# Kernel optimization log

Measured on AMD Instinct MI355X. Metric: run time of the kernel, lower is better.

The kernel has to match this reference:

```python
import jax, jax.numpy as jnp
import numpy as np
from jax import lax

N_NODES = 100000
N_EDGES = 6400000


def setup_inputs() -> dict:
    key = jax.random.key(0)
    k1, k2, k3, k4 = jax.random.split(key, 4)
    values = jax.random.uniform(k1, (N_NODES,), dtype=jnp.float32)
    edge_weights = jax.random.normal(k2, (N_EDGES,), dtype=jnp.float32)
    neighbor_idx = jax.random.randint(k3, (N_EDGES,), 0, N_NODES, dtype=jnp.int64 if jax.config.jax_enable_x64 else jnp.int32)
    segment_ids = jnp.sort(jax.random.randint(k4, (N_EDGES,), 0, N_NODES, dtype=jnp.int64 if jax.config.jax_enable_x64 else jnp.int32))
    return {
        "values": values,
        "edge_weights": edge_weights,
        "neighbor_idx": neighbor_idx,
        "segment_ids": segment_ids,
        "n_times": 3,
    }


def reference(values, edge_weights, neighbor_idx, segment_ids, n_times):
    # One forward_once: for each node i, new[i] = sigmoid(sum_{e: dst(e)=i} w_e * values[src(e)])
    # (per-node Linear(num_links, 1, bias=False) + Sigmoid, flattened over the ragged edge list)
    n_nodes = values.shape[0]

    def step(v, _):
        msgs = edge_weights * v[neighbor_idx]                      # [n_edges]
        agg = jax.ops.segment_sum(msgs, segment_ids, num_segments=n_nodes)
        return jax.nn.sigmoid(agg), None

    out, _ = lax.scan(step, values, None, length=int(n_times))
    return out
```

## Files before the change

kernel.cpp:

```cpp
#include <hip/hip_runtime.h>
#include <hip/hip_bf16.h>

#define BLK    512
#define EPT    16
#define CHUNK  24576
#define NPASS  5
#define CAP    (NPASS * CHUNK)
#define ROUNDS 6
#define SLOTS  640

__device__ __forceinline__ ushort f32_to_bf16_rne(float f) {
    unsigned u = __float_as_uint(f);
    unsigned r = (u + 0x7fffu + ((u >> 16) & 1u)) >> 16;
    return (ushort)r;
}

__global__ __launch_bounds__(BLK) void ppgcn_step(const ushort* __restrict__ vb,
                                                  const float* __restrict__ w,
                                                  const int* __restrict__ idx,
                                                  const int* __restrict__ seg,
                                                  float* __restrict__ acc,
                                                  int n_edges, int n_nodes) {
    __shared__ __align__(16) ushort chunk[CHUNK];
    __shared__ float slots[SLOTS];
    __shared__ int s_first, s_last;

    const int tid = threadIdx.x;
    const long long bstart = (long long)blockIdx.x * (BLK * EPT);
    const long long base   = bstart + (long long)tid * EPT;

    int ii[EPT]; float ww[EPT]; int ss[EPT];

    if (base + EPT <= (long long)n_edges) {
        const int4*   ip = reinterpret_cast<const int4*>(idx + base);
        const float4* wp = reinterpret_cast<const float4*>(w + base);
        const int4*   sp = reinterpret_cast<const int4*>(seg + base);
        #pragma unroll
        for (int q = 0; q < EPT / 4; ++q) {
            int4 a = ip[q]; float4 b = wp[q]; int4 c = sp[q];
            ii[4*q+0]=a.x; ii[4*q+1]=a.y; ii[4*q+2]=a.z; ii[4*q+3]=a.w;
            ww[4*q+0]=b.x; ww[4*q+1]=b.y; ww[4*q+2]=b.z; ww[4*q+3]=b.w;
            ss[4*q+0]=c.x; ss[4*q+1]=c.y; ss[4*q+2]=c.z; ss[4*q+3]=c.w;
        }
    } else {
        #pragma unroll
        for (int j = 0; j < EPT; ++j) {
            long long e = base + j;
            bool v = e < (long long)n_edges;
            ii[j] = v ? idx[e] : 0x7fffffff;
            ww[j] = v ? w[e]   : 0.0f;
            ss[j] = v ? seg[e] : 0x7fffffff;
        }
    }

    for (int s = tid; s < SLOTS; s += BLK) slots[s] = 0.0f;
    if (tid == 0) s_first = ss[0];
    {
        long long lastE = ((bstart + BLK * EPT) < (long long)n_edges ?
                           (bstart + BLK * EPT) : (long long)n_edges) - 1;
        int rel   = (int)(lastE - bstart);
        int owner = rel / EPT;
        int jl    = rel % EPT;
        if (tid == owner) s_last = ss[jl];
    }
    __syncthreads();
    const int first = s_first;

    unsigned long long slp = 0ull;
    int r = 0;
    int n0 = ss[0], n1 = -1, n2 = -1, n3 = -1;
    #pragma unroll
    for (int j = 1; j < EPT; ++j) {
        if (ss[j] != ss[j-1]) {
            r = (r < 7) ? r + 1 : 7;
            if      (r == 1) n1 = ss[j];
            else if (r == 2) n2 = ss[j];
            else if (r == 3) n3 = ss[j];
        }
        slp |= (unsigned long long)(unsigned)r << (3 * j);
    }

    float a0 = 0.f, a1 = 0.f, a2 = 0.f, a3 = 0.f;

    for (int p = 0; p < NPASS; ++p) {
        __syncthreads();
        const char* gsrc = (const char*)vb + (size_t)p * (CHUNK * 2);
        #pragma unroll
        for (int rr = 0; rr < ROUNDS; ++rr) {
            int off = (rr * BLK + tid) * 16;
            __builtin_amdgcn_global_load_lds(
                (const __attribute__((address_space(1))) void*)(gsrc + off),
                (__attribute__((address_space(3))) void*)((char*)chunk + off),
                16, 0, 0);
        }
        __syncthreads();

        const unsigned lo = (unsigned)(p * CHUNK);
        #pragma unroll
        for (int j = 0; j < EPT; ++j) {
            unsigned rel = (unsigned)ii[j] - lo;
            if (rel < (unsigned)CHUNK) {
                unsigned u = (unsigned)chunk[rel] << 16;
                float val = ww[j] * __uint_as_float(u);
                int sl = (int)((slp >> (3 * j)) & 7ull);
                a0 += (sl == 0) ? val : 0.0f;
                a1 += (sl == 1) ? val : 0.0f;
                a2 += (sl == 2) ? val : 0.0f;
                a3 += (sl == 3) ? val : 0.0f;
                if (sl >= 4) {
                    unsigned rs = (unsigned)(ss[j] - first);
                    if (rs < (unsigned)SLOTS) atomicAdd(&slots[rs], val);
                    else                      unsafeAtomicAdd(&acc[ss[j]], val);
                }
            }
        }
    }

    {
        int   nn[4] = { n0, n1, n2, n3 };
        float aa[4] = { a0, a1, a2, a3 };
        #pragma unroll
        for (int q = 0; q < 4; ++q) {
            int n = nn[q];
            if (n >= 0 && n < n_nodes) {
                unsigned rs = (unsigned)(n - first);
                if (rs < (unsigned)SLOTS) atomicAdd(&slots[rs], aa[q]);
                else                      unsafeAtomicAdd(&acc[n], aa[q]);
            }
        }
    }
    __syncthreads();

    {
        const int last = s_last;
        const int span = last - first;
        for (int s = tid; s <= span && s < SLOTS; s += BLK) {
            float v = slots[s];
            int node = first + s;
            if (s == 0 || node == last) unsafeAtomicAdd(&acc[node], v);
            else                        acc[node] = v;
        }
    }
}

__global__ __launch_bounds__(256) void ppgcn_convert(const float* __restrict__ src,
                                                     ushort* __restrict__ dst,
                                                     int n, int cap) {
    int i = blockIdx.x * 256 + threadIdx.x;
    if (i < cap) dst[i] = (i < n) ? f32_to_bf16_rne(src[i]) : (ushort)0;
}

__global__ __launch_bounds__(256) void ppgcn_sigmoid(float* __restrict__ acc,
                                                     ushort* __restrict__ bfout,
                                                     float* __restrict__ fout,
                                                     int n, int cap, int write_f32) {
    int i = blockIdx.x * 256 + threadIdx.x;
    if (i >= cap) return;
    if (i < n) {
        float a = acc[i];
        float s = 1.0f / (1.0f + expf(-a));
        bfout[i] = f32_to_bf16_rne(s);
        if (write_f32) fout[i] = s;
        acc[i] = 0.0f;
    } else {
        bfout[i] = 0;
    }
}

extern "C" void kernel_launch(void* const* d_in, const int* in_sizes, int n_in,
                              void* d_out, int out_size, void* d_ws, size_t ws_size,
                              hipStream_t stream) {
    const float* values       = (const float*)d_in[0];
    const float* edge_weights = (const float*)d_in[1];
    const int*   neighbor_idx = (const int*)d_in[2];
    const int*   segment_ids  = (const int*)d_in[3];

    const int n_nodes = in_sizes[0];
    const int n_edges = in_sizes[1];

    char* ws = (char*)d_ws;
    size_t abytes = ((size_t)n_nodes * sizeof(float) + 255) & ~(size_t)255;
    size_t vbytes = ((size_t)CAP * sizeof(ushort) + 255) & ~(size_t)255;
    float*  acc = (float*)ws;
    ushort* vb0 = (ushort*)(ws + abytes);
    ushort* vb1 = (ushort*)(ws + abytes + vbytes);
    ushort* vb2 = (ushort*)(ws + abytes + 2 * vbytes);
    float*  out = (float*)d_out;

    hipMemsetAsync(acc, 0, (size_t)n_nodes * sizeof(float), stream);

    int eblocks = (int)(((long long)n_edges + BLK * EPT - 1) / (BLK * EPT));
    int cblocks = (CAP + 255) / 256;

    ppgcn_convert<<<cblocks, 256, 0, stream>>>(values, vb0, n_nodes, CAP);

    ppgcn_step<<<eblocks, BLK, 0, stream>>>(vb0, edge_weights, neighbor_idx,
                                            segment_ids, acc, n_edges, n_nodes);
    ppgcn_sigmoid<<<cblocks, 256, 0, stream>>>(acc, vb1, out, n_nodes, CAP, 0);

    ppgcn_step<<<eblocks, BLK, 0, stream>>>(vb1, edge_weights, neighbor_idx,
                                            segment_ids, acc, n_edges, n_nodes);
    ppgcn_sigmoid<<<cblocks, 256, 0, stream>>>(acc, vb2, out, n_nodes, CAP, 0);

    ppgcn_step<<<eblocks, BLK, 0, stream>>>(vb2, edge_weights, neighbor_idx,
                                            segment_ids, acc, n_edges, n_nodes);
    ppgcn_sigmoid<<<cblocks, 256, 0, stream>>>(acc, vb0, out, n_nodes, CAP, 1);
}
```

Before: 140.8 us.

## Double-buffer LDS value chunks and defer segment reduction until after gathers

Splits the bf16 value table into smaller chunks held in two LDS buffers, issuing the async global-to-LDS load of the next chunk while the current one is gathered from. This removes one barrier per pass and hides load latency. Gathered products are now stored per edge and reduced by segment in a single run-length pass at the end, replacing the four-slot predicated accumulators. Edges per thread are halved, which doubles the block count and raises the number of chunk passes each block makes.

```diff
diff --git a/kernel.cpp b/kernel.cpp
--- a/kernel.cpp
+++ b/kernel.cpp
@@ -2,11 +2,11 @@
 #include <hip/hip_bf16.h>
 
 #define BLK    512
-#define EPT    16
-#define CHUNK  24576
-#define NPASS  5
+#define EPT    8
+#define CHUNK  12288
+#define NPASS  9
 #define CAP    (NPASS * CHUNK)
-#define ROUNDS 6
+#define ROUNDS 3
 #define SLOTS  640
 
 __device__ __forceinline__ ushort f32_to_bf16_rne(float f) {
@@ -21,7 +21,7 @@
                                                   const int* __restrict__ seg,
                                                   float* __restrict__ acc,
                                                   int n_edges, int n_nodes) {
-    __shared__ __align__(16) ushort chunk[CHUNK];
+    __shared__ __align__(16) ushort chunk[2][CHUNK];
     __shared__ float slots[SLOTS];
     __shared__ int s_first, s_last;
 
@@ -63,70 +63,75 @@
         int jl    = rel % EPT;
         if (tid == owner) s_last = ss[jl];
     }
-    __syncthreads();
-    const int first = s_first;
-
-    unsigned long long slp = 0ull;
-    int r = 0;
-    int n0 = ss[0], n1 = -1, n2 = -1, n3 = -1;
+
+    float g[EPT];
     #pragma unroll
-    for (int j = 1; j < EPT; ++j) {
-        if (ss[j] != ss[j-1]) {
-            r = (r < 7) ? r + 1 : 7;
-            if      (r == 1) n1 = ss[j];
-            else if (r == 2) n2 = ss[j];
-            else if (r == 3) n3 = ss[j];
-        }
-        slp |= (unsigned long long)(unsigned)r << (3 * j);
-    }
-
-    float a0 = 0.f, a1 = 0.f, a2 = 0.f, a3 = 0.f;
-
-    for (int p = 0; p < NPASS; ++p) {
-        __syncthreads();
-        const char* gsrc = (const char*)vb + (size_t)p * (CHUNK * 2);
+    for (int j = 0; j < EPT; ++j) g[j] = 0.0f;
+
+    {
+        const char* gsrc = (const char*)vb;
+        char* ldst = (char*)chunk[0];
         #pragma unroll
         for (int rr = 0; rr < ROUNDS; ++rr) {
             int off = (rr * BLK + tid) * 16;
             __builtin_amdgcn_global_load_lds(
                 (const __attribute__((address_space(1))) void*)(gsrc + off),
-                (__attribute__((address_space(3))) void*)((char*)chunk + off),
+                (__attribute__((address_space(3))) void*)(ldst + off),
                 16, 0, 0);
         }
-        __syncthreads();
+    }
+    __syncthreads();
+    const int first = s_first;
+
+    int cur = 0;
+    for (int p = 0; p < NPASS; ++p) {
+        if (p + 1 < NPASS) {
+            const char* gsrc = (const char*)vb + (size_t)(p + 1) * (CHUNK * 2);
+            char* ldst = (char*)chunk[cur ^ 1];
+            #pragma unroll
+            for (int rr = 0; rr < ROUNDS; ++rr) {
+                int off = (rr * BLK + tid) * 16;
+                __builtin_amdgcn_global_load_lds(
+                    (const __attribute__((address_space(1))) void*)(gsrc + off),
+                    (__attribute__((address_space(3))) void*)(ldst + off),
+                    16, 0, 0);
+            }
+        }
 
         const unsigned lo = (unsigned)(p * CHUNK);
+        const ushort* cbuf = chunk[cur];
         #pragma unroll
         for (int j = 0; j < EPT; ++j) {
             unsigned rel = (unsigned)ii[j] - lo;
             if (rel < (unsigned)CHUNK) {
-                unsigned u = (unsigned)chunk[rel] << 16;
-                float val = ww[j] * __uint_as_float(u);
-                int sl = (int)((slp >> (3 * j)) & 7ull);
-                a0 += (sl == 0) ? val : 0.0f;
-                a1 += (sl == 1) ? val : 0.0f;
-                a2 += (sl == 2) ? val : 0.0f;
-                a3 += (sl == 3) ? val : 0.0f;
-                if (sl >= 4) {
-                    unsigned rs = (unsigned)(ss[j] - first);
-                    if (rs < (unsigned)SLOTS) atomicAdd(&slots[rs], val);
-                    else                      unsafeAtomicAdd(&acc[ss[j]], val);
+                unsigned u = (unsigned)cbuf[rel] << 16;
+                g[j] = ww[j] * __uint_as_float(u);
+            }
+        }
+
+        __syncthreads();
+        cur ^= 1;
+    }
+
+    {
+        float run = g[0]; int cn = ss[0];
+        #pragma unroll
+        for (int j = 1; j < EPT; ++j) {
+            if (ss[j] != cn) {
+                if ((unsigned)cn < (unsigned)n_nodes) {
+                    unsigned rs = (unsigned)(cn - first);
+                    if (rs < (unsigned)SLOTS) atomicAdd(&slots[rs], run);
+                    else                      unsafeAtomicAdd(&acc[cn], run);
                 }
+                cn = ss[j]; run = g[j];
+            } else {
+                run += g[j];
             }
         }
-    }
-
-    {
-        int   nn[4] = { n0, n1, n2, n3 };
-        float aa[4] = { a0, a1, a2, a3 };
-        #pragma unroll
-        for (int q = 0; q < 4; ++q) {
-            int n = nn[q];
-            if (n >= 0 && n < n_nodes) {
-                unsigned rs = (unsigned)(n - first);
-                if (rs < (unsigned)SLOTS) atomicAdd(&slots[rs], aa[q]);
-                else                      unsafeAtomicAdd(&acc[n], aa[q]);
-            }
+        if ((unsigned)cn < (unsigned)n_nodes) {
+            unsigned rs = (unsigned)(cn - first);
+            if (rs < (unsigned)SLOTS) atomicAdd(&slots[rs], run);
+            else                      unsafeAtomicAdd(&acc[cn], run);
         }
     }
     __syncthreads();
```

After: 132.1 us. 1.07x faster.
